# Performance work log

Measured on AMD Instinct MI355X. Metric: run time of the kernel, lower is better.

Reference implementation:

```python
import jax, jax.numpy as jnp
import numpy as np

N_NODES = 100000
D = 128
N_EDGES = 640000


def _spmm(edge_index, w, x, n):
    # out[i] = sum over edges (i<-j): w * x[j]
    src, dst = edge_index[0], edge_index[1]
    return jax.ops.segment_sum(w[:, None] * x[dst], src, num_segments=n)


def setup_inputs() -> dict:
    key = jax.random.key(0)
    ks = jax.random.split(key, 8)
    inp = {
        "index_vectors": jax.random.normal(ks[0], (N_NODES, D), dtype=jnp.float32),
        "edge_index1": jax.random.randint(ks[1], (2, N_EDGES), 0, N_NODES, dtype=jnp.int64),
        "w1": jnp.ones((N_EDGES,), dtype=jnp.float32),
        "edge_index2": jax.random.randint(ks[2], (2, N_EDGES), 0, N_NODES, dtype=jnp.int64),
        "w2": jnp.ones((N_EDGES,), dtype=jnp.float32),
        "edge_index3": jax.random.randint(ks[3], (2, N_EDGES), 0, N_NODES, dtype=jnp.int64),
        "w3": jnp.ones((N_EDGES,), dtype=jnp.float32),
        "zeroth": jax.random.uniform(ks[4], (1, 1), dtype=jnp.float32),
        "fst": jax.random.uniform(ks[5], (1, 1), dtype=jnp.float32),
        "snd": jax.random.uniform(ks[6], (1, 1), dtype=jnp.float32),
        "trd": jax.random.uniform(ks[7], (1, 1), dtype=jnp.float32),
    }
    return inp


def reference(index_vectors, edge_index1, w1, edge_index2, w2, edge_index3, w3,
              zeroth, fst, snd, trd):
    n = index_vectors.shape[0]
    # hop-1 context: A @ x
    fst_ctx = _spmm(edge_index1, w1, index_vectors, n)
    # hop-2 context: A^2 @ roll(x, 1, axis=1)   (permute_vecs=True)
    snd_ctx = _spmm(edge_index2, w2, jnp.roll(index_vectors, 1, axis=1), n)
    # hop-3 context: A^3 @ roll(x, 2, axis=1)
    trd_ctx = _spmm(edge_index3, w3, jnp.roll(index_vectors, 2, axis=1), n)

    # relu-normalized scalar order weights (get_orders)
    r0, r1, r2, r3 = (jax.nn.relu(zeroth), jax.nn.relu(fst),
                      jax.nn.relu(snd), jax.nn.relu(trd))
    tot = r0 + r1 + r2 + r3 + 1e-6
    r0, r1, r2, r3 = r0 / tot, r1 / tot, r2 / tot, r3 / tot

    # use_sign=False -> plain weighted combination
    return r0 * index_vectors + r1 * fst_ctx + r2 * snd_ctx + r3 * trd_ctx
```

## Files before the change

### kernel.cpp

```cpp
#include <hip/hip_runtime.h>

#define N_NODES 100000
#define D 128
#define N_EDGES 640000
#define TOT_EDGES (3 * N_EDGES)

#define NB   1024
#define NPB  98
#define BCAP 2304
#define RPT  9
#define OVF_CAP 16384
#define EPB  2560
#define BINA_BLOCKS (TOT_EDGES / EPB)
#define BLK_PER_SET (N_EDGES / EPB)
#define EPT  (EPB / 256)
#define NKEY 512
#define CAST_BLOCKS ((N_NODES * D / 4 + 255) / 256)

#define WS_OVFCNT 0
#define WS_BCUR   64
#define WS_OVF    65600
#define WS_TMP    327744
#define WS_FREC   19202112
#define WS_OFFS   34562112
#define WS_XB     34962120
#define WS_TOTAL_FAST 60562120

#ifndef __has_builtin
#define __has_builtin(x) 0
#endif
#if __has_builtin(__builtin_amdgcn_alignbit)
#define ALIGN16(hi, lo) __builtin_amdgcn_alignbit((hi), (lo), 16)
#else
#define ALIGN16(hi, lo) (((hi) << 16) | ((lo) >> 16))
#endif

__device__ __forceinline__ void load_r(const float* z0, const float* z1,
                                       const float* z2, const float* z3,
                                       float& r0, float& r1, float& r2, float& r3) {
    r0 = fmaxf(z0[0], 0.0f);
    r1 = fmaxf(z1[0], 0.0f);
    r2 = fmaxf(z2[0], 0.0f);
    r3 = fmaxf(z3[0], 0.0f);
    float inv = 1.0f / (r0 + r1 + r2 + r3 + 1e-6f);
    r0 *= inv; r1 *= inv; r2 *= inv; r3 *= inv;
}

__device__ __forceinline__ unsigned short bf16rn(float f) {
    unsigned int u = __float_as_uint(f);
    u += 0x7FFFu + ((u >> 16) & 1u);
    return (unsigned short)(u >> 16);
}

__global__ __launch_bounds__(256) void prep_kernel(
        const float* __restrict__ x, ushort* __restrict__ xb,
        const int* __restrict__ ei1, const float* __restrict__ w1,
        const int* __restrict__ ei2, const float* __restrict__ w2,
        const int* __restrict__ ei3, const float* __restrict__ w3,
        const float* __restrict__ z0, const float* __restrict__ z1,
        const float* __restrict__ z2, const float* __restrict__ z3,
        int* __restrict__ bcur, int* __restrict__ ovf_count,
        int4* __restrict__ ovf, int2* __restrict__ tmp) {
    if (blockIdx.x >= BINA_BLOCKS) {
        int i = (blockIdx.x - BINA_BLOCKS) * 256 + threadIdx.x;
        if (i < N_NODES * D / 4) {
            float4 v = ((const float4*)x)[i];
            ushort4 h;
            h.x = bf16rn(v.x); h.y = bf16rn(v.y); h.z = bf16rn(v.z); h.w = bf16rn(v.w);
            ((ushort4*)xb)[i] = h;
        }
        return;
    }
    __shared__ int hist[NB];
    __shared__ int base[NB];
    int t = threadIdx.x;
    for (int i = t; i < NB; i += 256) hist[i] = 0;
    __syncthreads();

    float r0, r1, r2, r3;
    load_r(z0, z1, z2, z3, r0, r1, r2, r3);

    int set = blockIdx.x / BLK_PER_SET;
    int e0  = (blockIdx.x - set * BLK_PER_SET) * EPB;
    const int* ei;  const float* w;  float rk;
    if      (set == 0) { ei = ei1; w = w1; rk = r1; }
    else if (set == 1) { ei = ei2; w = w2; rk = r2; }
    else               { ei = ei3; w = w3; rk = r3; }

    int rank[EPT];
    int bkt[EPT];
    int rxv[EPT];
    float scv[EPT];

#pragma unroll
    for (int k = 0; k < EPT; ++k) {
        int idx = e0 + t + k * 256;
        int src = ei[idx];
        int dst = ei[N_EDGES + idx];
        int b = src / NPB;
        int local = src - b * NPB;
        bkt[k]  = b;
        rxv[k]  = dst | (set << 17) | (local << 19);
        scv[k]  = rk * w[idx];
        rank[k] = atomicAdd(&hist[b], 1);
    }
    __syncthreads();

    for (int i = t; i < NB; i += 256) {
        int h = hist[i];
        base[i] = h ? atomicAdd(&bcur[i * 16], h) : 0;
    }
    __syncthreads();

#pragma unroll
    for (int k = 0; k < EPT; ++k) {
        int b = bkt[k];
        int pos = base[b] + rank[k];
        if (pos < BCAP) {
            tmp[(size_t)b * BCAP + pos] = make_int2(rxv[k], __float_as_int(scv[k]));
        } else {
            int o = atomicAdd(ovf_count, 1);
            int src = b * NPB + ((rxv[k] >> 19) & 0x7F);
            if (o < OVF_CAP) ovf[o] = make_int4(src, rxv[k] & 0x7FFFF,
                                                __float_as_int(scv[k]), 0);
        }
    }
}

#define GB_ACC(V, RX, SC)                                                      \
    {                                                                          \
        int sh = ((RX) >> 17) & 3;                                             \
        unsigned int pw = (unsigned int)__shfl((int)(V).w, prevq);             \
        unsigned int s1x = ALIGN16((V).x, pw);                                 \
        unsigned int s1y = ALIGN16((V).y, (V).x);                              \
        unsigned int s1z = ALIGN16((V).z, (V).y);                              \
        unsigned int s1w = ALIGN16((V).w, (V).z);                              \
        unsigned int u0 = (sh == 0) ? (V).x : (sh == 1) ? s1x : pw;            \
        unsigned int u1 = (sh == 0) ? (V).y : (sh == 1) ? s1y : (V).x;         \
        unsigned int u2 = (sh == 0) ? (V).z : (sh == 1) ? s1z : (V).y;         \
        unsigned int u3 = (sh == 0) ? (V).w : (sh == 1) ? s1w : (V).z;         \
        acc0 += (SC) * __uint_as_float(u0 << 16);                              \
        acc1 += (SC) * __uint_as_float(u0 & 0xFFFF0000u);                      \
        acc2 += (SC) * __uint_as_float(u1 << 16);                              \
        acc3 += (SC) * __uint_as_float(u1 & 0xFFFF0000u);                      \
        acc4 += (SC) * __uint_as_float(u2 << 16);                              \
        acc5 += (SC) * __uint_as_float(u2 & 0xFFFF0000u);                      \
        acc6 += (SC) * __uint_as_float(u3 << 16);                              \
        acc7 += (SC) * __uint_as_float(u3 & 0xFFFF0000u);                      \
    }

__global__ __launch_bounds__(256) void gfuse_kernel(
        const float* __restrict__ x, const ushort* __restrict__ xb,
        const int* __restrict__ bcur, const int2* __restrict__ tmp,
        const float* __restrict__ z0, const float* __restrict__ z1,
        const float* __restrict__ z2, const float* __restrict__ z3,
        float* __restrict__ out) {
    __shared__ int2 srecs[BCAP];
    __shared__ int d[NKEY];
    __shared__ int ts[256];
    __shared__ int cur[NKEY];
    __shared__ int nodebeg[NPB + 1];

    int b = blockIdx.x;
    int t = threadIdx.x;

    int n = bcur[b * 16];
    if (n > BCAP) n = BCAP;

    int   mrx[RPT];
    int   mry[RPT];
#pragma unroll
    for (int k = 0; k < RPT; ++k) {
        int i = t + k * 256;
        if (i < n) {
            int2 rec = tmp[(size_t)b * BCAP + i];
            mrx[k] = rec.x; mry[k] = rec.y;
        } else {
            mrx[k] = -1; mry[k] = 0;
        }
    }

    d[t] = 0; d[t + 256] = 0;
    __syncthreads();
#pragma unroll
    for (int k = 0; k < RPT; ++k) {
        if (mrx[k] != -1) {
            int key = (((mrx[k] >> 19) & 0x7F) << 2) | ((mrx[k] >> 17) & 3);
            atomicAdd(&d[key], 1);
        }
    }
    __syncthreads();

    int k0 = d[2 * t], k1 = d[2 * t + 1];
    int tot = k0 + k1;
    ts[t] = tot;
    __syncthreads();
    for (int off = 1; off < 256; off <<= 1) {
        int v = (t >= off) ? ts[t - off] : 0;
        __syncthreads();
        ts[t] += v;
        __syncthreads();
    }
    int tbase = ts[t] - tot;
    cur[2 * t]     = tbase;
    cur[2 * t + 1] = tbase + k0;
    __syncthreads();

    if (t < NPB) nodebeg[t] = cur[t << 2];
    if (t == NPB) nodebeg[NPB] = n;
    __syncthreads();

#pragma unroll
    for (int k = 0; k < RPT; ++k) {
        if (mrx[k] != -1) {
            int key = (((mrx[k] >> 19) & 0x7F) << 2) | ((mrx[k] >> 17) & 3);
            int pos = atomicAdd(&cur[key], 1);
            srecs[pos] = make_int2(mrx[k], mry[k]);
        }
    }
    __syncthreads();

    float r0, r1, r2, r3;
    load_r(z0, z1, z2, z3, r0, r1, r2, r3);

    int wv    = t >> 6;
    int lane  = t & 63;
    int qt    = lane >> 4;
    int l16   = lane & 15;
    int prevq = (qt << 4) | ((l16 + 15) & 15);

    for (int l = wv; l < NPB; l += 4) {
        int node = b * NPB + l;
        if (node >= N_NODES) break;
        int beg = nodebeg[l];
        int cnt = nodebeg[l + 1] - beg;

        float acc0 = 0.f, acc1 = 0.f, acc2 = 0.f, acc3 = 0.f;
        float acc4 = 0.f, acc5 = 0.f, acc6 = 0.f, acc7 = 0.f;

        for (int j = 0; j < cnt; j += 4) {
            int o = j + qt;
            bool ok = o < cnt;
            int2 rec = srecs[beg + (ok ? o : 0)];
            int rx = rec.x;
            float sc = ok ? __int_as_float(rec.y) : 0.f;
            const uint4* rowp = (const uint4*)(xb + (size_t)(rx & 0x1FFFF) * D);
            uint4 v = rowp[l16];
            GB_ACC(v, rx, sc)
        }

        acc0 += __shfl_xor(acc0, 16); acc0 += __shfl_xor(acc0, 32);
        acc1 += __shfl_xor(acc1, 16); acc1 += __shfl_xor(acc1, 32);
        acc2 += __shfl_xor(acc2, 16); acc2 += __shfl_xor(acc2, 32);
        acc3 += __shfl_xor(acc3, 16); acc3 += __shfl_xor(acc3, 32);
        acc4 += __shfl_xor(acc4, 16); acc4 += __shfl_xor(acc4, 32);
        acc5 += __shfl_xor(acc5, 16); acc5 += __shfl_xor(acc5, 32);
        acc6 += __shfl_xor(acc6, 16); acc6 += __shfl_xor(acc6, 32);
        acc7 += __shfl_xor(acc7, 16); acc7 += __shfl_xor(acc7, 32);

        if (lane < 16) {
            const float4* xr = (const float4*)(x + (size_t)node * D);
            float4 xlo = xr[2 * l16];
            float4 xhi = xr[2 * l16 + 1];
            float4 olo, ohi;
            olo.x = r0 * xlo.x + acc0;
            olo.y = r0 * xlo.y + acc1;
            olo.z = r0 * xlo.z + acc2;
            olo.w = r0 * xlo.w + acc3;
            ohi.x = r0 * xhi.x + acc4;
            ohi.y = r0 * xhi.y + acc5;
            ohi.z = r0 * xhi.z + acc6;
            ohi.w = r0 * xhi.w + acc7;
            float4* op = (float4*)(out + (size_t)node * D);
            op[2 * l16]     = olo;
            op[2 * l16 + 1] = ohi;
        }
    }
}

__global__ void ovf_kernel(const float* __restrict__ x,
                           const int* __restrict__ ovf_count,
                           const int4* __restrict__ ovf,
                           float* __restrict__ out) {
    int total_waves = (gridDim.x * blockDim.x) >> 6;
    int gw   = (blockIdx.x * blockDim.x + threadIdx.x) >> 6;
    int lane = threadIdx.x & 63;
    int n = *ovf_count;
    if (n > OVF_CAP) n = OVF_CAP;
    for (int r = gw; r < n; r += total_waves) {
        int4 rec = ovf[r];
        int src = rec.x;
        int dst = rec.y & 0x1FFFF;
        int sh  = (rec.y >> 17) & 3;
        float sc = __int_as_float(rec.z);
        const float* xr = x + (size_t)dst * D;
        float* orow = out + (size_t)src * D;
        int c0 = 2 * lane, c1 = 2 * lane + 1;
        atomicAdd(&orow[c0], sc * xr[(c0 - sh) & 127]);
        atomicAdd(&orow[c1], sc * xr[(c1 - sh) & 127]);
    }
}

#define SCAN_BLOCKS ((N_NODES + 255) / 256)
#define WS_COUNTS   0
#define WS_OFFSETS  400000
#define WS_CURSORS  800008
#define WS_BSUM     1200008
#define WS_BPRE     1201576
#define WS_RECS     1203144
#define WS_NEEDED_MID (WS_RECS + (size_t)TOT_EDGES * 8)

__global__ void hist_kernel(const int* __restrict__ ei1, const int* __restrict__ ei2,
                            const int* __restrict__ ei3, int* __restrict__ counts) {
    int e = blockIdx.x * blockDim.x + threadIdx.x;
    if (e >= TOT_EDGES) return;
    int set = e / N_EDGES;
    int idx = e - set * N_EDGES;
    const int* ei = (set == 0) ? ei1 : (set == 1) ? ei2 : ei3;
    atomicAdd(&counts[ei[idx]], 1);
}

__global__ void scan1_kernel(const int* __restrict__ counts,
                             int* __restrict__ offsets, int* __restrict__ bsum) {
    __shared__ int s[256];
    int t = threadIdx.x;
    int i = blockIdx.x * 256 + t;
    int v = (i < N_NODES) ? counts[i] : 0;
    s[t] = v;
    __syncthreads();
    for (int off = 1; off < 256; off <<= 1) {
        int u = (t >= off) ? s[t - off] : 0;
        __syncthreads();
        s[t] += u;
        __syncthreads();
    }
    if (i < N_NODES) offsets[i] = s[t] - v;
    if (t == 255) bsum[blockIdx.x] = s[255];
}

__global__ void scan2_kernel(const int* __restrict__ bsum, int* __restrict__ bpre) {
    __shared__ int s[512];
    int t = threadIdx.x;
    int v = (t < SCAN_BLOCKS) ? bsum[t] : 0;
    s[t] = v;
    __syncthreads();
    for (int off = 1; off < 512; off <<= 1) {
        int u = (t >= off) ? s[t - off] : 0;
        __syncthreads();
        s[t] += u;
        __syncthreads();
    }
    if (t < SCAN_BLOCKS) bpre[t] = s[t] - v;
}

__global__ void scan3_kernel(int* __restrict__ offsets, const int* __restrict__ bpre,
                             int* __restrict__ cursors) {
    int i = blockIdx.x * 256 + threadIdx.x;
    if (i < N_NODES) {
        int v = offsets[i] + bpre[blockIdx.x];
        offsets[i] = v;
        cursors[i] = v;
    }
    if (i == 0) offsets[N_NODES] = TOT_EDGES;
}

__global__ void fill_kernel(const int* __restrict__ ei1, const float* __restrict__ w1,
                            const int* __restrict__ ei2, const float* __restrict__ w2,
                            const int* __restrict__ ei3, const float* __restrict__ w3,
                            const float* __restrict__ z0, const float* __restrict__ z1,
                            const float* __restrict__ z2, const float* __restrict__ z3,
                            int* __restrict__ cursors, int2* __restrict__ recs) {
    int e = blockIdx.x * blockDim.x + threadIdx.x;
    if (e >= TOT_EDGES) return;
    int set = e / N_EDGES;
    int idx = e - set * N_EDGES;
    const int* ei;  const float* w;
    if      (set == 0) { ei = ei1; w = w1; }
    else if (set == 1) { ei = ei2; w = w2; }
    else               { ei = ei3; w = w3; }
    float r0, r1, r2, r3;
    load_r(z0, z1, z2, z3, r0, r1, r2, r3);
    float rk = (set == 0) ? r1 : (set == 1) ? r2 : r3;
    int src = ei[idx];
    int dst = ei[N_EDGES + idx];
    float scale = rk * w[idx];
    int pos = atomicAdd(&cursors[src], 1);
    recs[pos] = make_int2(dst | (set << 17), __float_as_int(scale));
}

__global__ void gatherd_kernel(const float* __restrict__ x,
                               const int* __restrict__ offsets,
                               const int2* __restrict__ recs,
                               const float* __restrict__ z0, const float* __restrict__ z1,
                               const float* __restrict__ z2, const float* __restrict__ z3,
                               float* __restrict__ out) {
    int wid  = (blockIdx.x * blockDim.x + threadIdx.x) >> 6;
    int lane = threadIdx.x & 63;
    if (wid >= N_NODES) return;
    float r0, r1, r2, r3;
    load_r(z0, z1, z2, z3, r0, r1, r2, r3);
    float2 xv = ((const float2*)(x + (size_t)wid * D))[lane];
    int beg = offsets[wid];
    int end = offsets[wid + 1];
    float2 a0 = {0.f, 0.f}, a1 = {0.f, 0.f}, a2 = {0.f, 0.f};
    for (int j = beg; j < end; ++j) {
        int2 rec = recs[j];
        float2 v = ((const float2*)(x + (size_t)(rec.x & 0x1FFFF) * D))[lane];
        int sh = (rec.x >> 17) & 3;
        float sc = __int_as_float(rec.y);
        if      (sh == 0) { a0.x += sc * v.x; a0.y += sc * v.y; }
        else if (sh == 1) { a1.x += sc * v.x; a1.y += sc * v.y; }
        else               { a2.x += sc * v.x; a2.y += sc * v.y; }
    }
    int prev = (lane + 63) & 63;
    float r1y = __shfl(a1.y, prev);
    float r2x = __shfl(a2.x, prev);
    float r2y = __shfl(a2.y, prev);
    float2 o;
    o.x = r0 * xv.x + a0.x + r1y  + r2x;
    o.y = r0 * xv.y + a0.y + a1.x + r2y;
    ((float2*)(out + (size_t)wid * D))[lane] = o;
}

extern "C" void kernel_launch(void* const* d_in, const int* in_sizes, int n_in,
                              void* d_out, int out_size, void* d_ws, size_t ws_size,
                              hipStream_t stream) {
    const float* x   = (const float*)d_in[0];
    const int*   ei1 = (const int*)  d_in[1];
    const float* w1  = (const float*)d_in[2];
    const int*   ei2 = (const int*)  d_in[3];
    const float* w2  = (const float*)d_in[4];
    const int*   ei3 = (const int*)  d_in[5];
    const float* w3  = (const float*)d_in[6];
    const float* z0  = (const float*)d_in[7];
    const float* z1  = (const float*)d_in[8];
    const float* z2  = (const float*)d_in[9];
    const float* z3  = (const float*)d_in[10];
    float* out = (float*)d_out;
    char* wsc = (char*)d_ws;

    if (ws_size >= WS_TOTAL_FAST) {
        int*    ovf_count = (int*)   (wsc + WS_OVFCNT);
        int*    bcur      = (int*)   (wsc + WS_BCUR);
        int4*   ovf       = (int4*)  (wsc + WS_OVF);
        int2*   tmp       = (int2*)  (wsc + WS_TMP);
        ushort* xb        = (ushort*)(wsc + WS_XB);

        hipMemsetAsync(wsc, 0, WS_OVF, stream);
        prep_kernel<<<BINA_BLOCKS + CAST_BLOCKS, 256, 0, stream>>>(
            x, xb, ei1, w1, ei2, w2, ei3, w3, z0, z1, z2, z3,
            bcur, ovf_count, ovf, tmp);
        gfuse_kernel<<<NB, 256, 0, stream>>>(x, xb, bcur, tmp,
                                             z0, z1, z2, z3, out);
        ovf_kernel<<<128, 256, 0, stream>>>(x, ovf_count, ovf, out);
    } else {
        int*  counts  = (int*) (wsc + WS_COUNTS);
        int*  offsets = (int*) (wsc + WS_OFFSETS);
        int*  cursors = (int*) (wsc + WS_CURSORS);
        int*  bsum    = (int*) (wsc + WS_BSUM);
        int*  bpre    = (int*) (wsc + WS_BPRE);
        int2* recs    = (int2*)(wsc + WS_RECS);

        hipMemsetAsync(counts, 0, N_NODES * sizeof(int), stream);
        hist_kernel<<<TOT_EDGES / 256, 256, 0, stream>>>(ei1, ei2, ei3, counts);
        scan1_kernel<<<SCAN_BLOCKS, 256, 0, stream>>>(counts, offsets, bsum);
        scan2_kernel<<<1, 512, 0, stream>>>(bsum, bpre);
        scan3_kernel<<<SCAN_BLOCKS, 256, 0, stream>>>(offsets, bpre, cursors);
        fill_kernel<<<TOT_EDGES / 256, 256, 0, stream>>>(ei1, w1, ei2, w2, ei3, w3,
                                                         z0, z1, z2, z3, cursors, recs);
        gatherd_kernel<<<(N_NODES * 64 + 255) / 256, 256, 0, stream>>>(x, offsets, recs,
                                                                       z0, z1, z2, z3, out);
    }
}
```

Baseline: 284.2 us.

## Split bf16 feature gather into column slices with halo for cache locality

The bf16 copy of x is relaid out as 8 column slices of 36 bytes per node, each with one extra leading word so rolled columns can be read without cross-lane shuffles. The old fused kernel is split into a bin-sort kernel that writes sorted records and per-node offsets and counts back to global memory, and a gather kernel whose blocks each handle 16 nodes for one slice. The aim is a small per-slice working set (3.6 MB) that stays cache-resident for the random gathers. In exchange, every edge record is re-read once per slice, there is an extra launch and a global round trip for the sorted records, and there are more accumulators and shuffles.

```diff
diff --git a/kernel.cpp b/kernel.cpp
--- a/kernel.cpp
+++ b/kernel.cpp
@@ -15,25 +15,24 @@
 #define BLK_PER_SET (N_EDGES / EPB)
 #define EPT  (EPB / 256)
 #define NKEY 512
-#define CAST_BLOCKS ((N_NODES * D / 4 + 255) / 256)
+
+#define NSL  8
+#define SLW  16
+#define SLB  36
+#define SLICE_BYTES ((size_t)N_NODES * SLB)
+
+#define SCAST_BLOCKS (N_NODES / 4)
+#define NPG  16
+#define GATHER_BLOCKS ((N_NODES / NPG) * NSL)
 
 #define WS_OVFCNT 0
 #define WS_BCUR   64
 #define WS_OVF    65600
 #define WS_TMP    327744
-#define WS_FREC   19202112
-#define WS_OFFS   34562112
-#define WS_XB     34962120
-#define WS_TOTAL_FAST 60562120
-
-#ifndef __has_builtin
-#define __has_builtin(x) 0
-#endif
-#if __has_builtin(__builtin_amdgcn_alignbit)
-#define ALIGN16(hi, lo) __builtin_amdgcn_alignbit((hi), (lo), 16)
-#else
-#define ALIGN16(hi, lo) (((hi) << 16) | ((lo) >> 16))
-#endif
+#define WS_OFFS   19202112
+#define WS_CNTS   19602112
+#define WS_XB3    20002112
+#define WS_TOTAL_FAST 48802112
 
 __device__ __forceinline__ void load_r(const float* z0, const float* z1,
                                        const float* z2, const float* z3,
@@ -53,7 +52,7 @@
 }
 
 __global__ __launch_bounds__(256) void prep_kernel(
-        const float* __restrict__ x, ushort* __restrict__ xb,
+        const float* __restrict__ x, char* __restrict__ xb3,
         const int* __restrict__ ei1, const float* __restrict__ w1,
         const int* __restrict__ ei2, const float* __restrict__ w2,
         const int* __restrict__ ei3, const float* __restrict__ w3,
@@ -62,12 +61,19 @@
         int* __restrict__ bcur, int* __restrict__ ovf_count,
         int4* __restrict__ ovf, int2* __restrict__ tmp) {
     if (blockIdx.x >= BINA_BLOCKS) {
-        int i = (blockIdx.x - BINA_BLOCKS) * 256 + threadIdx.x;
-        if (i < N_NODES * D / 4) {
-            float4 v = ((const float4*)x)[i];
-            ushort4 h;
-            h.x = bf16rn(v.x); h.y = bf16rn(v.y); h.z = bf16rn(v.z); h.w = bf16rn(v.w);
-            ((ushort4*)xb)[i] = h;
+        int c    = blockIdx.x - BINA_BLOCKS;
+        int w    = threadIdx.x >> 6;
+        int lane = threadIdx.x & 63;
+        int node = c * 4 + w;
+        float2 xv = ((const float2*)(x + (size_t)node * D))[lane];
+        unsigned int vd = ((unsigned int)bf16rn(xv.y) << 16) | (unsigned int)bf16rn(xv.x);
+        int d  = lane;
+        int s1 = d >> 3;
+        *(unsigned int*)(xb3 + (size_t)s1 * SLICE_BYTES + (size_t)node * SLB
+                         + (size_t)(((d & 7) + 1) << 2)) = vd;
+        if ((d & 7) == 7) {
+            int s2 = (s1 + 1) & 7;
+            *(unsigned int*)(xb3 + (size_t)s2 * SLICE_BYTES + (size_t)node * SLB) = vd;
         }
         return;
     }
@@ -127,71 +133,38 @@
     }
 }
 
-#define GB_ACC(V, RX, SC)                                                      \
-    {                                                                          \
-        int sh = ((RX) >> 17) & 3;                                             \
-        unsigned int pw = (unsigned int)__shfl((int)(V).w, prevq);             \
-        unsigned int s1x = ALIGN16((V).x, pw);                                 \
-        unsigned int s1y = ALIGN16((V).y, (V).x);                              \
-        unsigned int s1z = ALIGN16((V).z, (V).y);                              \
-        unsigned int s1w = ALIGN16((V).w, (V).z);                              \
-        unsigned int u0 = (sh == 0) ? (V).x : (sh == 1) ? s1x : pw;            \
-        unsigned int u1 = (sh == 0) ? (V).y : (sh == 1) ? s1y : (V).x;         \
-        unsigned int u2 = (sh == 0) ? (V).z : (sh == 1) ? s1z : (V).y;         \
-        unsigned int u3 = (sh == 0) ? (V).w : (sh == 1) ? s1w : (V).z;         \
-        acc0 += (SC) * __uint_as_float(u0 << 16);                              \
-        acc1 += (SC) * __uint_as_float(u0 & 0xFFFF0000u);                      \
-        acc2 += (SC) * __uint_as_float(u1 << 16);                              \
-        acc3 += (SC) * __uint_as_float(u1 & 0xFFFF0000u);                      \
-        acc4 += (SC) * __uint_as_float(u2 << 16);                              \
-        acc5 += (SC) * __uint_as_float(u2 & 0xFFFF0000u);                      \
-        acc6 += (SC) * __uint_as_float(u3 << 16);                              \
-        acc7 += (SC) * __uint_as_float(u3 & 0xFFFF0000u);                      \
-    }
-
-__global__ __launch_bounds__(256) void gfuse_kernel(
-        const float* __restrict__ x, const ushort* __restrict__ xb,
-        const int* __restrict__ bcur, const int2* __restrict__ tmp,
-        const float* __restrict__ z0, const float* __restrict__ z1,
-        const float* __restrict__ z2, const float* __restrict__ z3,
-        float* __restrict__ out) {
-    __shared__ int2 srecs[BCAP];
-    __shared__ int d[NKEY];
+__global__ __launch_bounds__(256) void binB_kernel(
+        const int* __restrict__ bcur, int2* __restrict__ tmp,
+        int* __restrict__ offs, int* __restrict__ cnts) {
+    __shared__ int dH[NKEY];
     __shared__ int ts[256];
     __shared__ int cur[NKEY];
-    __shared__ int nodebeg[NPB + 1];
-
+    __shared__ int nb[NPB + 1];
     int b = blockIdx.x;
     int t = threadIdx.x;
-
     int n = bcur[b * 16];
     if (n > BCAP) n = BCAP;
 
-    int   mrx[RPT];
-    int   mry[RPT];
+    int mrx[RPT], mry[RPT];
 #pragma unroll
     for (int k = 0; k < RPT; ++k) {
         int i = t + k * 256;
-        if (i < n) {
-            int2 rec = tmp[(size_t)b * BCAP + i];
-            mrx[k] = rec.x; mry[k] = rec.y;
-        } else {
-            mrx[k] = -1; mry[k] = 0;
-        }
-    }
-
-    d[t] = 0; d[t + 256] = 0;
+        if (i < n) { int2 r = tmp[(size_t)b * BCAP + i]; mrx[k] = r.x; mry[k] = r.y; }
+        else       { mrx[k] = -1; mry[k] = 0; }
+    }
+
+    dH[t] = 0; dH[t + 256] = 0;
     __syncthreads();
 #pragma unroll
     for (int k = 0; k < RPT; ++k) {
         if (mrx[k] != -1) {
             int key = (((mrx[k] >> 19) & 0x7F) << 2) | ((mrx[k] >> 17) & 3);
-            atomicAdd(&d[key], 1);
-        }
-    }
-    __syncthreads();
-
-    int k0 = d[2 * t], k1 = d[2 * t + 1];
+            atomicAdd(&dH[key], 1);
+        }
+    }
+    __syncthreads();
+
+    int k0 = dH[2 * t], k1 = dH[2 * t + 1];
     int tot = k0 + k1;
     ts[t] = tot;
     __syncthreads();
@@ -201,13 +174,12 @@
         ts[t] += v;
         __syncthreads();
     }
-    int tbase = ts[t] - tot;
-    cur[2 * t]     = tbase;
-    cur[2 * t + 1] = tbase + k0;
-    __syncthreads();
-
-    if (t < NPB) nodebeg[t] = cur[t << 2];
-    if (t == NPB) nodebeg[NPB] = n;
+    int tb = ts[t] - tot;
+    cur[2 * t]     = tb;
+    cur[2 * t + 1] = tb + k0;
+    __syncthreads();
+
+    if (t <= NPB) nb[t] = (t < NPB) ? cur[t << 2] : n;
     __syncthreads();
 
 #pragma unroll
@@ -215,65 +187,94 @@
         if (mrx[k] != -1) {
             int key = (((mrx[k] >> 19) & 0x7F) << 2) | ((mrx[k] >> 17) & 3);
             int pos = atomicAdd(&cur[key], 1);
-            srecs[pos] = make_int2(mrx[k], mry[k]);
-        }
-    }
-    __syncthreads();
+            tmp[(size_t)b * BCAP + pos] = make_int2(mrx[k], mry[k]);
+        }
+    }
+
+    if (t < NPB) {
+        int node = b * NPB + t;
+        if (node < N_NODES) {
+            offs[node] = b * BCAP + nb[t];
+            cnts[node] = nb[t + 1] - nb[t];
+        }
+    }
+}
+
+__global__ __launch_bounds__(256) void gslice_kernel(
+        const float* __restrict__ x, const char* __restrict__ xb3,
+        const int* __restrict__ offs, const int* __restrict__ cnts,
+        const int2* __restrict__ tmp,
+        const float* __restrict__ z0, const float* __restrict__ z1,
+        const float* __restrict__ z2, const float* __restrict__ z3,
+        float* __restrict__ out) {
+    int s  = blockIdx.x & 7;
+    int ng = blockIdx.x >> 3;
+    int w    = threadIdx.x >> 6;
+    int lane = threadIdx.x & 63;
+    int g = lane >> 3;
+    int l = lane & 7;
+    const char* xs = xb3 + (size_t)s * SLICE_BYTES;
+    int c0 = s * SLW;
 
     float r0, r1, r2, r3;
     load_r(z0, z1, z2, z3, r0, r1, r2, r3);
 
-    int wv    = t >> 6;
-    int lane  = t & 63;
-    int qt    = lane >> 4;
-    int l16   = lane & 15;
-    int prevq = (qt << 4) | ((l16 + 15) & 15);
-
-    for (int l = wv; l < NPB; l += 4) {
-        int node = b * NPB + l;
-        if (node >= N_NODES) break;
-        int beg = nodebeg[l];
-        int cnt = nodebeg[l + 1] - beg;
-
-        float acc0 = 0.f, acc1 = 0.f, acc2 = 0.f, acc3 = 0.f;
-        float acc4 = 0.f, acc5 = 0.f, acc6 = 0.f, acc7 = 0.f;
-
-        for (int j = 0; j < cnt; j += 4) {
-            int o = j + qt;
-            bool ok = o < cnt;
-            int2 rec = srecs[beg + (ok ? o : 0)];
-            int rx = rec.x;
-            float sc = ok ? __int_as_float(rec.y) : 0.f;
-            const uint4* rowp = (const uint4*)(xb + (size_t)(rx & 0x1FFFF) * D);
-            uint4 v = rowp[l16];
-            GB_ACC(v, rx, sc)
-        }
-
-        acc0 += __shfl_xor(acc0, 16); acc0 += __shfl_xor(acc0, 32);
-        acc1 += __shfl_xor(acc1, 16); acc1 += __shfl_xor(acc1, 32);
-        acc2 += __shfl_xor(acc2, 16); acc2 += __shfl_xor(acc2, 32);
-        acc3 += __shfl_xor(acc3, 16); acc3 += __shfl_xor(acc3, 32);
-        acc4 += __shfl_xor(acc4, 16); acc4 += __shfl_xor(acc4, 32);
-        acc5 += __shfl_xor(acc5, 16); acc5 += __shfl_xor(acc5, 32);
-        acc6 += __shfl_xor(acc6, 16); acc6 += __shfl_xor(acc6, 32);
-        acc7 += __shfl_xor(acc7, 16); acc7 += __shfl_xor(acc7, 32);
-
-        if (lane < 16) {
-            const float4* xr = (const float4*)(x + (size_t)node * D);
-            float4 xlo = xr[2 * l16];
-            float4 xhi = xr[2 * l16 + 1];
-            float4 olo, ohi;
-            olo.x = r0 * xlo.x + acc0;
-            olo.y = r0 * xlo.y + acc1;
-            olo.z = r0 * xlo.z + acc2;
-            olo.w = r0 * xlo.w + acc3;
-            ohi.x = r0 * xhi.x + acc4;
-            ohi.y = r0 * xhi.y + acc5;
-            ohi.z = r0 * xhi.z + acc6;
-            ohi.w = r0 * xhi.w + acc7;
-            float4* op = (float4*)(out + (size_t)node * D);
-            op[2 * l16]     = olo;
-            op[2 * l16 + 1] = ohi;
+    unsigned int loff = (unsigned int)(l << 2);
+
+    for (int ni = 0; ni < NPG / 4; ++ni) {
+        int node = ng * NPG + w + ni * 4;
+        int beg = offs[node];
+        int cnt = cnts[node];
+
+        float A0x = 0.f, A0y = 0.f, A1x = 0.f, A1y = 0.f, A2x = 0.f, A2y = 0.f;
+        float X0 = 0.f, X1 = 0.f, X2 = 0.f;
+
+        for (int j = 0; j < cnt; j += 8) {
+            int q = j + g;
+            int ii = beg + ((q < cnt) ? q : cnt - 1);
+            const int* rp = (const int*)(tmp + ii);
+            int rx = __builtin_nontemporal_load(rp);
+            int ry = __builtin_nontemporal_load(rp + 1);
+            float sc = (q < cnt) ? __int_as_float(ry) : 0.f;
+            int dst = rx & 0x1FFFF;
+            int sh  = (rx >> 17) & 3;
+            unsigned int boff = (unsigned int)dst * 36u;
+            unsigned int u  = *(const unsigned int*)(xs + boff + loff);
+            unsigned int u8 = *(const unsigned int*)(xs + boff + 32u);
+            float lo  = __uint_as_float(u << 16);
+            float hi  = __uint_as_float(u & 0xFFFF0000u);
+            float lo8 = __uint_as_float(u8 << 16);
+            float hi8 = __uint_as_float(u8 & 0xFFFF0000u);
+            float m0 = (sh == 0) ? sc : 0.f;
+            float m1 = (sh == 1) ? sc : 0.f;
+            float m2 = (sh == 2) ? sc : 0.f;
+            A0x += m0 * lo;  A0y += m0 * hi;
+            A1x += m1 * lo;  A1y += m1 * hi;
+            A2x += m2 * lo;  A2y += m2 * hi;
+            X0  += m0 * lo8; X1  += m0 * hi8; X2 += m1 * lo8;
+        }
+
+        float M0 = (l == 0) ? X0 : A0x;
+        float M1 = (l == 0) ? X1 : A0y;
+        float M2 = (l == 0) ? X2 : A1x;
+        int sl = (lane & 56) | ((l + 1) & 7);
+        float va = __shfl(M0, sl);
+        float vb = __shfl(M1, sl);
+        float vc = __shfl(M2, sl);
+        float oe = va + A1y + A2x;
+        float oo = vb + vc + A2y;
+
+        oe += __shfl_xor(oe, 8);  oo += __shfl_xor(oo, 8);
+        oe += __shfl_xor(oe, 16); oo += __shfl_xor(oo, 16);
+        oe += __shfl_xor(oe, 32); oo += __shfl_xor(oo, 32);
+
+        if (g == 0) {
+            const float* xp = x + (size_t)node * D + c0 + 2 * l;
+            float xe = __builtin_nontemporal_load(xp);
+            float xo = __builtin_nontemporal_load(xp + 1);
+            float* op = out + (size_t)node * D + c0 + 2 * l;
+            __builtin_nontemporal_store(r0 * xe + oe, op);
+            __builtin_nontemporal_store(r0 * xo + oo, op + 1);
         }
     }
 }
@@ -440,18 +441,21 @@
     char* wsc = (char*)d_ws;
 
     if (ws_size >= WS_TOTAL_FAST) {
-        int*    ovf_count = (int*)   (wsc + WS_OVFCNT);
-        int*    bcur      = (int*)   (wsc + WS_BCUR);
-        int4*   ovf       = (int4*)  (wsc + WS_OVF);
-        int2*   tmp       = (int2*)  (wsc + WS_TMP);
-        ushort* xb        = (ushort*)(wsc + WS_XB);
+        int*  ovf_count = (int*) (wsc + WS_OVFCNT);
+        int*  bcur      = (int*) (wsc + WS_BCUR);
+        int4* ovf       = (int4*)(wsc + WS_OVF);
+        int2* tmp       = (int2*)(wsc + WS_TMP);
+        int*  offs      = (int*) (wsc + WS_OFFS);
+        int*  cnts      = (int*) (wsc + WS_CNTS);
+        char* xb3       =        (wsc + WS_XB3);
 
         hipMemsetAsync(wsc, 0, WS_OVF, stream);
-        prep_kernel<<<BINA_BLOCKS + CAST_BLOCKS, 256, 0, stream>>>(
-            x, xb, ei1, w1, ei2, w2, ei3, w3, z0, z1, z2, z3,
+        prep_kernel<<<BINA_BLOCKS + SCAST_BLOCKS, 256, 0, stream>>>(
+            x, xb3, ei1, w1, ei2, w2, ei3, w3, z0, z1, z2, z3,
             bcur, ovf_count, ovf, tmp);
-        gfuse_kernel<<<NB, 256, 0, stream>>>(x, xb, bcur, tmp,
-                                             z0, z1, z2, z3, out);
+        binB_kernel<<<NB, 256, 0, stream>>>(bcur, tmp, offs, cnts);
+        gslice_kernel<<<GATHER_BLOCKS, 256, 0, stream>>>(x, xb3, offs, cnts, tmp,
+                                                         z0, z1, z2, z3, out);
         ovf_kernel<<<128, 256, 0, stream>>>(x, ovf_count, ovf, out);
     } else {
         int*  counts  = (int*) (wsc + WS_COUNTS);
```

Measured after the change: 626.1 us. +120.3%, slower.
